# Kernel tuning notes

Measured on AMD Instinct MI355X. Metric: run time of the kernel, lower is better.

## Reference

```python
import jax, jax.numpy as jnp
import numpy as np


def setup_inputs() -> dict:
    key = jax.random.key(0)
    ks = jax.random.split(key, 16)
    B, S, L2 = 16, 1024, 2048

    def rn(k, shape, scale=0.1):
        return jax.random.normal(k, shape, dtype=jnp.float32) * scale

    return {
        "x": rn(ks[0], (B, S, 3), 1.0),
        "v1": rn(ks[1], (B, L2 + 1, 3), 1.0),
        "v2": rn(ks[2], (B, L2 + 1, 3), 1.0),
        # Attention: Linear(6, 1)
        "attn_w": rn(ks[3], (1, 6)),
        "attn_b": rn(ks[4], (1,)),
        # fc1: Linear(3, 16)
        "fc1_w": rn(ks[5], (16, 3)),
        "fc1_b": rn(ks[6], (16,)),
        # LSTM(16, 32, 1), gate order i,f,g,o -> 4*32 = 128
        "w_ih": rn(ks[7], (128, 16)),
        "w_hh": rn(ks[8], (128, 32)),
        "b_ih": rn(ks[9], (128,)),
        "b_hh": rn(ks[10], (128,)),
        # fc2: Linear(38, 16)
        "fc2_w": rn(ks[11], (16, 38)),
        "fc2_b": rn(ks[12], (16,)),
        # fc3: Linear(16, 3)
        "fc3_w": rn(ks[13], (3, 16)),
        "fc3_b": rn(ks[14], (3,)),
    }


def _attention(x, v, attn_w, attn_b):
    # Linear(6,1) over cat([x_i, key_j]) decomposes into x-part + key-part,
    # avoiding the original [B,S,L2,6] repeat/cat intermediate (same math).
    key_, value = v[:, :-1], v[:, 1:]          # [B,L2,3] each
    wx, wk = attn_w[0, :3], attn_w[0, 3:]
    scores = (x @ wx)[:, :, None] + (key_ @ wk)[:, None, :] + attn_b[0]  # [B,S,L2]
    a = jax.nn.softmax(scores, axis=-1)
    return jnp.einsum('bij,bjd->bid', a, value)  # [B,S,3]


def _lstm(x, w_ih, w_hh, b_ih, b_hh):
    # Single-layer batch_first LSTM, zero initial state, pytorch gate order i,f,g,o.
    B = x.shape[0]
    H = w_hh.shape[1]
    xg = x @ w_ih.T + (b_ih + b_hh)  # [B,S,4H] precomputed input contribution

    def step(carry, g_t):
        h, c = carry
        g = g_t + h @ w_hh.T
        i, f, gg, o = jnp.split(g, 4, axis=-1)
        c = jax.nn.sigmoid(f) * c + jax.nn.sigmoid(i) * jnp.tanh(gg)
        h = jax.nn.sigmoid(o) * jnp.tanh(c)
        return (h, c), h

    init = (jnp.zeros((B, H), x.dtype), jnp.zeros((B, H), x.dtype))
    _, hs = jax.lax.scan(step, init, jnp.swapaxes(xg, 0, 1))  # [S,B,H]
    return jnp.swapaxes(hs, 0, 1)  # [B,S,H]


def reference(x, v1, v2, attn_w, attn_b, fc1_w, fc1_b,
              w_ih, w_hh, b_ih, b_hh, fc2_w, fc2_b, fc3_w, fc3_b):
    a1 = _attention(x, v1, attn_w, attn_b)   # [B,S,3]
    a2 = _attention(x, v2, attn_w, attn_b)   # [B,S,3]
    h = _lstm(x @ fc1_w.T + fc1_b, w_ih, w_hh, b_ih, b_hh)  # [B,S,32]
    cat = jnp.concatenate([a1, a2, h], axis=-1)              # [B,S,38]
    out = jax.nn.relu(cat @ fc2_w.T + fc2_b) @ fc3_w.T + fc3_b
    return out  # [B,S,3]
```

## Files before the change

### kernel.cpp

```cpp
#include <hip/hip_runtime.h>
#include <hip/hip_bf16.h>

#define B_ 16
#define S_ 1024
#define L_ 2048
#define H_ 32

typedef float f2v __attribute__((ext_vector_type(2)));
typedef float f4v __attribute__((ext_vector_type(4)));

static __device__ __forceinline__ f2v pkfma(f2v a, f2v b, f2v c) {
    f2v d;
    asm("v_pk_fma_f32 %0, %1, %2, %3" : "=v"(d) : "v"(a), "v"(b), "v"(c));
    return d;
}
static __device__ __forceinline__ f2v pkadd(f2v a, f2v b) {
    f2v d;
    asm("v_pk_add_f32 %0, %1, %2" : "=v"(d) : "v"(a), "v"(b));
    return d;
}

__global__ __launch_bounds__(64) void fused_attn_lstm(
    const float* __restrict__ x,
    const float* __restrict__ v1,
    const float* __restrict__ v2,
    const float* __restrict__ attn_w,
    const float* __restrict__ fc1_w,
    const float* __restrict__ fc1_b,
    const float* __restrict__ w_ih,
    const float* __restrict__ w_hh,
    const float* __restrict__ b_ih,
    const float* __restrict__ b_hh,
    float* __restrict__ A,
    float* __restrict__ h_out)
{
    const int blk = blockIdx.x;
    const int l   = threadIdx.x;

    if (blk >= 16) {
        const int idx = blk - 16;
        const int b = idx & 15, sel = idx >> 4;
        const float* v = (sel ? v2 : v1) + (size_t)b * ((L_ + 1) * 3);
        const float wk0 = attn_w[3], wk1 = attn_w[4], wk2 = attn_w[5];

        float s[32];
        float mx = -3.4e38f;
#pragma unroll
        for (int k = 0; k < 32; ++k) {
            const float* p = v + (l + (k << 6)) * 3;
            float sc = fmaf(p[2], wk2, fmaf(p[1], wk1, p[0] * wk0));
            s[k] = sc; mx = fmaxf(mx, sc);
        }
#pragma unroll
        for (int o = 1; o < 64; o <<= 1) mx = fmaxf(mx, __shfl_xor(mx, o));

        float den = 0.f, a0 = 0.f, a1 = 0.f, a2 = 0.f;
#pragma unroll
        for (int k = 0; k < 32; ++k) {
            float e = __expf(s[k] - mx);
            const float* p = v + (l + (k << 6) + 1) * 3;
            den += e;
            a0 = fmaf(e, p[0], a0); a1 = fmaf(e, p[1], a1); a2 = fmaf(e, p[2], a2);
        }
#pragma unroll
        for (int o = 1; o < 64; o <<= 1) {
            den += __shfl_xor(den, o); a0 += __shfl_xor(a0, o);
            a1  += __shfl_xor(a1, o);  a2 += __shfl_xor(a2, o);
        }
        if (l == 0) {
            float inv = 1.0f / den;
            float* dst = A + sel * 48 + b * 3;
            dst[0] = a0 * inv; dst[1] = a1 * inv; dst[2] = a2 * inv;
        }
        return;
    }

    const int b  = blk;
    const int j  = l & 31;
    const int hi = l >> 5;
    const int r0 = hi ? (32 + j) : j;
    const int r1 = hi ? (96 + j) : (64 + j);

    __shared__ float lds_x[S_ * 3];
    __shared__ float lds_h[64];

    {
        const f4v* src = (const f4v*)(x + (size_t)b * (S_ * 3));
        f4v* dst = (f4v*)lds_x;
#pragma unroll
        for (int m = 0; m < 12; ++m) dst[l + 64 * m] = src[l + 64 * m];
    }
    if (l < 32) lds_h[l] = 0.f;

    f2v wh0[16], wh1[16];
    {
        const f4v* p0 = (const f4v*)(w_hh + r0 * H_);
        const f4v* p1 = (const f4v*)(w_hh + r1 * H_);
#pragma unroll
        for (int m = 0; m < 8; ++m) {
            f4v a = p0[m];
            wh0[2*m]   = __builtin_shufflevector(a, a, 0, 1);
            wh0[2*m+1] = __builtin_shufflevector(a, a, 2, 3);
            f4v c2 = p1[m];
            wh1[2*m]   = __builtin_shufflevector(c2, c2, 0, 1);
            wh1[2*m+1] = __builtin_shufflevector(c2, c2, 2, 3);
        }
    }

    float W00 = 0, W01 = 0, W02 = 0, W10 = 0, W11 = 0, W12 = 0, bb0, bb1;
    {
        float s0 = 0, s1 = 0;
#pragma unroll
        for (int k = 0; k < 16; ++k) {
            float wi0 = w_ih[r0 * 16 + k], wi1 = w_ih[r1 * 16 + k];
            float f0 = fc1_w[k * 3 + 0], f1 = fc1_w[k * 3 + 1], f2 = fc1_w[k * 3 + 2];
            float fb = fc1_b[k];
            W00 = fmaf(wi0, f0, W00); W01 = fmaf(wi0, f1, W01); W02 = fmaf(wi0, f2, W02);
            s0  = fmaf(wi0, fb, s0);
            W10 = fmaf(wi1, f0, W10); W11 = fmaf(wi1, f1, W11); W12 = fmaf(wi1, f2, W12);
            s1  = fmaf(wi1, fb, s1);
        }
        bb0 = s0 + b_ih[r0] + b_hh[r0];
        bb1 = s1 + b_ih[r1] + b_hh[r1];
    }

    const float CE = -1.44269504f;
    const float c1 = hi ? CE : 2.f * CE;
    float c = 0.f;
    float* hob = h_out + ((size_t)b << 15);

#define STEP(T, RB, WB) do {                                                          \
        float x0 = lds_x[3*(T)], x1 = lds_x[3*(T)+1], x2 = lds_x[3*(T)+2];            \
        f2v acc0a = { fmaf(W02,x2, fmaf(W01,x1, fmaf(W00,x0, bb0))), 0.f };           \
        f2v acc1a = { fmaf(W12,x2, fmaf(W11,x1, fmaf(W10,x0, bb1))), 0.f };           \
        f2v acc0b = { 0.f, 0.f };                                                     \
        f2v acc1b = { 0.f, 0.f };                                                     \
        _Pragma("unroll")                                                             \
        for (int m = 0; m < 8; ++m) {                                                 \
            f4v hv = *(const f4v*)&lds_h[(RB) + 4*m];                                 \
            f2v hlo = __builtin_shufflevector(hv, hv, 0, 1);                          \
            f2v hhi = __builtin_shufflevector(hv, hv, 2, 3);                          \
            acc0a = pkfma(wh0[2*m],   hlo, acc0a);                                    \
            acc1a = pkfma(wh1[2*m],   hlo, acc1a);                                    \
            acc0b = pkfma(wh0[2*m+1], hhi, acc0b);                                    \
            acc1b = pkfma(wh1[2*m+1], hhi, acc1b);                                    \
        }                                                                             \
        f2v acc0 = pkadd(acc0a, acc0b);                                               \
        f2v acc1 = pkadd(acc1a, acc1b);                                               \
        float a0 = acc0.x + acc0.y;                                                   \
        float a1 = acc1.x + acc1.y;                                                   \
        float s0 = __builtin_amdgcn_rcpf(1.f + __builtin_amdgcn_exp2f(a0 * CE));      \
        float s1 = __builtin_amdgcn_rcpf(1.f + __builtin_amdgcn_exp2f(a1 * c1));      \
        float t0 = __shfl_xor(s0, 32);                                                \
        float t1 = __shfl_xor(s1, 32);                                                \
        float si = hi ? t0 : s0;                                                      \
        float sf = hi ? s0 : t0;                                                      \
        float sg = hi ? t1 : s1;                                                      \
        float so = hi ? s1 : t1;                                                      \
        float tg = fmaf(2.f, sg, -1.f);                                               \
        c = fmaf(sf, c, si * tg);                                                     \
        float tc = fmaf(2.f, __builtin_amdgcn_rcpf(1.f + __builtin_amdgcn_exp2f(c * (2.f*CE))), -1.f); \
        float hval = so * tc;                                                         \
        if (!hi) lds_h[(WB) + j] = hval;                                              \
        else     hob[((T) << 5) + j] = hval;                                          \
    } while (0)

    for (int t = 0; t < S_; t += 2) {
        STEP(t,     0, 32);
        STEP(t + 1, 32, 0);
    }
#undef STEP
}

__global__ __launch_bounds__(256) void final_kernel(
    const float* __restrict__ h,
    const float* __restrict__ A,
    const float* __restrict__ fc2_w,
    const float* __restrict__ fc2_b,
    const float* __restrict__ fc3_w,
    const float* __restrict__ fc3_b,
    float* __restrict__ out)
{
    __shared__ float sw2[16 * 38], sb2[16], sw3[48], sb3[3], sA[96];
    const int tid = threadIdx.x;
    for (int i = tid; i < 16 * 38; i += 256) sw2[i] = fc2_w[i];
    if (tid < 96) sA[tid] = A[tid];
    if (tid < 16) sb2[tid] = fc2_b[tid];
    if (tid < 48) sw3[tid] = fc3_w[tid];
    if (tid < 3)  sb3[tid] = fc3_b[tid];
    __syncthreads();

    const int p = blockIdx.x * 256 + tid;
    if (p >= B_ * S_) return;
    const int b = p >> 10;

    float hv[32];
    {
        const float4* hp = (const float4*)(h + ((size_t)p << 5));
#pragma unroll
        for (int m = 0; m < 8; ++m) {
            float4 t = hp[m];
            hv[4*m] = t.x; hv[4*m+1] = t.y; hv[4*m+2] = t.z; hv[4*m+3] = t.w;
        }
    }
    const float a10 = sA[b*3+0], a11 = sA[b*3+1], a12 = sA[b*3+2];
    const float a20 = sA[48+b*3+0], a21 = sA[48+b*3+1], a22 = sA[48+b*3+2];

    float y[16];
#pragma unroll
    for (int u = 0; u < 16; ++u) {
        const float* w = sw2 + u * 38;
        float acc = sb2[u];
        acc = fmaf(w[0], a10, acc); acc = fmaf(w[1], a11, acc); acc = fmaf(w[2], a12, acc);
        acc = fmaf(w[3], a20, acc); acc = fmaf(w[4], a21, acc); acc = fmaf(w[5], a22, acc);
#pragma unroll
        for (int k = 0; k < 32; ++k) acc = fmaf(w[6 + k], hv[k], acc);
        y[u] = fmaxf(acc, 0.f);
    }
#pragma unroll
    for (int d = 0; d < 3; ++d) {
        float o = sb3[d];
#pragma unroll
        for (int u = 0; u < 16; ++u) o = fmaf(sw3[d * 16 + u], y[u], o);
        out[p * 3 + d] = o;
    }
}

extern "C" void kernel_launch(void* const* d_in, const int* in_sizes, int n_in,
                              void* d_out, int out_size, void* d_ws, size_t ws_size,
                              hipStream_t stream) {
    const float* x      = (const float*)d_in[0];
    const float* v1     = (const float*)d_in[1];
    const float* v2     = (const float*)d_in[2];
    const float* attn_w = (const float*)d_in[3];
    const float* fc1_w  = (const float*)d_in[5];
    const float* fc1_b  = (const float*)d_in[6];
    const float* w_ih   = (const float*)d_in[7];
    const float* w_hh   = (const float*)d_in[8];
    const float* b_ih   = (const float*)d_in[9];
    const float* b_hh   = (const float*)d_in[10];
    const float* fc2_w  = (const float*)d_in[11];
    const float* fc2_b  = (const float*)d_in[12];
    const float* fc3_w  = (const float*)d_in[13];
    const float* fc3_b  = (const float*)d_in[14];
    float* out = (float*)d_out;

    float* Aws = (float*)d_ws;
    float* hws = (float*)((char*)d_ws + 4096);

    fused_attn_lstm<<<48, 64, 0, stream>>>(x, v1, v2, attn_w, fc1_w, fc1_b,
                                           w_ih, w_hh, b_ih, b_hh, Aws, hws);
    final_kernel  <<<64, 256, 0, stream>>>(hws, Aws, fc2_w, fc2_b, fc3_w, fc3_b, out);
}
```

Before: 395.8 us.

## Fuse attention and output MLP into LSTM kernel, use permlane swap for gates

Merges the attention, LSTM and final MLP into one 16-block kernel, so the second launch and the attention workspace disappear. Each block now runs its two attention reductions and the fc2/fc3 epilogue after the recurrence. The log2e scaling is folded into the recurrent and input weights and biases, and the two cross-half shuffles per step become v_permlane32_swap. Both changes shorten the serial per-step dependency chain. The cost is that attention and the epilogue now run serially on only 16 wavefronts instead of in parallel blocks.

```diff
diff --git a/kernel.cpp b/kernel.cpp
--- a/kernel.cpp
+++ b/kernel.cpp
@@ -19,8 +19,11 @@
     asm("v_pk_add_f32 %0, %1, %2" : "=v"(d) : "v"(a), "v"(b));
     return d;
 }
-
-__global__ __launch_bounds__(64) void fused_attn_lstm(
+static __device__ __forceinline__ void pl32swap(float& a, float& b) {
+    asm("v_permlane32_swap_b32 %0, %1" : "+v"(a), "+v"(b));
+}
+
+__global__ __launch_bounds__(64) void fused_net(
     const float* __restrict__ x,
     const float* __restrict__ v1,
     const float* __restrict__ v2,
@@ -31,51 +34,15 @@
     const float* __restrict__ w_hh,
     const float* __restrict__ b_ih,
     const float* __restrict__ b_hh,
-    float* __restrict__ A,
-    float* __restrict__ h_out)
+    const float* __restrict__ fc2_w,
+    const float* __restrict__ fc2_b,
+    const float* __restrict__ fc3_w,
+    const float* __restrict__ fc3_b,
+    float* __restrict__ h_ws,
+    float* __restrict__ out)
 {
-    const int blk = blockIdx.x;
-    const int l   = threadIdx.x;
-
-    if (blk >= 16) {
-        const int idx = blk - 16;
-        const int b = idx & 15, sel = idx >> 4;
-        const float* v = (sel ? v2 : v1) + (size_t)b * ((L_ + 1) * 3);
-        const float wk0 = attn_w[3], wk1 = attn_w[4], wk2 = attn_w[5];
-
-        float s[32];
-        float mx = -3.4e38f;
-#pragma unroll
-        for (int k = 0; k < 32; ++k) {
-            const float* p = v + (l + (k << 6)) * 3;
-            float sc = fmaf(p[2], wk2, fmaf(p[1], wk1, p[0] * wk0));
-            s[k] = sc; mx = fmaxf(mx, sc);
-        }
-#pragma unroll
-        for (int o = 1; o < 64; o <<= 1) mx = fmaxf(mx, __shfl_xor(mx, o));
-
-        float den = 0.f, a0 = 0.f, a1 = 0.f, a2 = 0.f;
-#pragma unroll
-        for (int k = 0; k < 32; ++k) {
-            float e = __expf(s[k] - mx);
-            const float* p = v + (l + (k << 6) + 1) * 3;
-            den += e;
-            a0 = fmaf(e, p[0], a0); a1 = fmaf(e, p[1], a1); a2 = fmaf(e, p[2], a2);
-        }
-#pragma unroll
-        for (int o = 1; o < 64; o <<= 1) {
-            den += __shfl_xor(den, o); a0 += __shfl_xor(a0, o);
-            a1  += __shfl_xor(a1, o);  a2 += __shfl_xor(a2, o);
-        }
-        if (l == 0) {
-            float inv = 1.0f / den;
-            float* dst = A + sel * 48 + b * 3;
-            dst[0] = a0 * inv; dst[1] = a1 * inv; dst[2] = a2 * inv;
-        }
-        return;
-    }
-
-    const int b  = blk;
+    const int b  = blockIdx.x;
+    const int l  = threadIdx.x;
     const int j  = l & 31;
     const int hi = l >> 5;
     const int r0 = hi ? (32 + j) : j;
@@ -92,6 +59,9 @@
     }
     if (l < 32) lds_h[l] = 0.f;
 
+    const float CE = -1.44269504f;
+    const float k1 = hi ? CE : 2.f * CE;
+
     f2v wh0[16], wh1[16];
     {
         const f4v* p0 = (const f4v*)(w_hh + r0 * H_);
@@ -99,14 +69,13 @@
 #pragma unroll
         for (int m = 0; m < 8; ++m) {
             f4v a = p0[m];
-            wh0[2*m]   = __builtin_shufflevector(a, a, 0, 1);
-            wh0[2*m+1] = __builtin_shufflevector(a, a, 2, 3);
+            wh0[2*m]   = f2v{a.x * CE, a.y * CE};
+            wh0[2*m+1] = f2v{a.z * CE, a.w * CE};
             f4v c2 = p1[m];
-            wh1[2*m]   = __builtin_shufflevector(c2, c2, 0, 1);
-            wh1[2*m+1] = __builtin_shufflevector(c2, c2, 2, 3);
-        }
-    }
-
+            wh1[2*m]   = f2v{c2.x * k1, c2.y * k1};
+            wh1[2*m+1] = f2v{c2.z * k1, c2.w * k1};
+        }
+    }
     float W00 = 0, W01 = 0, W02 = 0, W10 = 0, W11 = 0, W12 = 0, bb0, bb1;
     {
         float s0 = 0, s1 = 0;
@@ -120,14 +89,14 @@
             W10 = fmaf(wi1, f0, W10); W11 = fmaf(wi1, f1, W11); W12 = fmaf(wi1, f2, W12);
             s1  = fmaf(wi1, fb, s1);
         }
-        bb0 = s0 + b_ih[r0] + b_hh[r0];
-        bb1 = s1 + b_ih[r1] + b_hh[r1];
-    }
-
-    const float CE = -1.44269504f;
-    const float c1 = hi ? CE : 2.f * CE;
+        bb0 = (s0 + b_ih[r0] + b_hh[r0]) * CE;
+        bb1 = (s1 + b_ih[r1] + b_hh[r1]) * k1;
+        W00 *= CE; W01 *= CE; W02 *= CE;
+        W10 *= k1; W11 *= k1; W12 *= k1;
+    }
+
     float c = 0.f;
-    float* hob = h_out + ((size_t)b << 15);
+    float* hob = h_ws + ((size_t)b << 15);
 
 #define STEP(T, RB, WB) do {                                                          \
         float x0 = lds_x[3*(T)], x1 = lds_x[3*(T)+1], x2 = lds_x[3*(T)+2];            \
@@ -147,16 +116,16 @@
         }                                                                             \
         f2v acc0 = pkadd(acc0a, acc0b);                                               \
         f2v acc1 = pkadd(acc1a, acc1b);                                               \
-        float a0 = acc0.x + acc0.y;                                                   \
-        float a1 = acc1.x + acc1.y;                                                   \
-        float s0 = __builtin_amdgcn_rcpf(1.f + __builtin_amdgcn_exp2f(a0 * CE));      \
-        float s1 = __builtin_amdgcn_rcpf(1.f + __builtin_amdgcn_exp2f(a1 * c1));      \
-        float t0 = __shfl_xor(s0, 32);                                                \
-        float t1 = __shfl_xor(s1, 32);                                                \
-        float si = hi ? t0 : s0;                                                      \
-        float sf = hi ? s0 : t0;                                                      \
-        float sg = hi ? t1 : s1;                                                      \
-        float so = hi ? s1 : t1;                                                      \
+        float s0 = __builtin_amdgcn_rcpf(1.f + __builtin_amdgcn_exp2f(acc0.x + acc0.y)); \
+        float s1 = __builtin_amdgcn_rcpf(1.f + __builtin_amdgcn_exp2f(acc1.x + acc1.y)); \
+        float A0 = s0, B0 = s1;                                                       \
+        pl32swap(A0, B0);                            \
+        float C0 = s1, D0 = s0;                                                       \
+        pl32swap(C0, D0);                            \
+        float si = hi ? C0 : s0;                                                      \
+        float sf = hi ? s0 : B0;                                                      \
+        float sg = hi ? A0 : s1;                                                      \
+        float so = hi ? s1 : D0;                                                      \
         float tg = fmaf(2.f, sg, -1.f);                                               \
         c = fmaf(sf, c, si * tg);                                                     \
         float tc = fmaf(2.f, __builtin_amdgcn_rcpf(1.f + __builtin_amdgcn_exp2f(c * (2.f*CE))), -1.f); \
@@ -170,59 +139,81 @@
         STEP(t + 1, 32, 0);
     }
 #undef STEP
-}
-
-__global__ __launch_bounds__(256) void final_kernel(
-    const float* __restrict__ h,
-    const float* __restrict__ A,
-    const float* __restrict__ fc2_w,
-    const float* __restrict__ fc2_b,
-    const float* __restrict__ fc3_w,
-    const float* __restrict__ fc3_b,
-    float* __restrict__ out)
-{
-    __shared__ float sw2[16 * 38], sb2[16], sw3[48], sb3[3], sA[96];
-    const int tid = threadIdx.x;
-    for (int i = tid; i < 16 * 38; i += 256) sw2[i] = fc2_w[i];
-    if (tid < 96) sA[tid] = A[tid];
-    if (tid < 16) sb2[tid] = fc2_b[tid];
-    if (tid < 48) sw3[tid] = fc3_w[tid];
-    if (tid < 3)  sb3[tid] = fc3_b[tid];
-    __syncthreads();
-
-    const int p = blockIdx.x * 256 + tid;
-    if (p >= B_ * S_) return;
-    const int b = p >> 10;
-
-    float hv[32];
-    {
-        const float4* hp = (const float4*)(h + ((size_t)p << 5));
-#pragma unroll
-        for (int m = 0; m < 8; ++m) {
-            float4 t = hp[m];
-            hv[4*m] = t.x; hv[4*m+1] = t.y; hv[4*m+2] = t.z; hv[4*m+3] = t.w;
-        }
-    }
-    const float a10 = sA[b*3+0], a11 = sA[b*3+1], a12 = sA[b*3+2];
-    const float a20 = sA[48+b*3+0], a21 = sA[48+b*3+1], a22 = sA[48+b*3+2];
-
-    float y[16];
-#pragma unroll
-    for (int u = 0; u < 16; ++u) {
-        const float* w = sw2 + u * 38;
-        float acc = sb2[u];
-        acc = fmaf(w[0], a10, acc); acc = fmaf(w[1], a11, acc); acc = fmaf(w[2], a12, acc);
-        acc = fmaf(w[3], a20, acc); acc = fmaf(w[4], a21, acc); acc = fmaf(w[5], a22, acc);
-#pragma unroll
-        for (int k = 0; k < 32; ++k) acc = fmaf(w[6 + k], hv[k], acc);
-        y[u] = fmaxf(acc, 0.f);
-    }
-#pragma unroll
-    for (int d = 0; d < 3; ++d) {
-        float o = sb3[d];
-#pragma unroll
-        for (int u = 0; u < 16; ++u) o = fmaf(sw3[d * 16 + u], y[u], o);
-        out[p * 3 + d] = o;
+
+    float a1v0, a1v1, a1v2, a2v0, a2v1, a2v2;
+    {
+        const float wk0 = attn_w[3], wk1 = attn_w[4], wk2 = attn_w[5];
+#pragma unroll
+        for (int sel = 0; sel < 2; ++sel) {
+            const float* v = (sel ? v2 : v1) + (size_t)b * ((L_ + 1) * 3);
+            float s[32];
+            float mx = -3.4e38f;
+#pragma unroll
+            for (int k = 0; k < 32; ++k) {
+                const float* p = v + (l + (k << 6)) * 3;
+                float sc = fmaf(p[2], wk2, fmaf(p[1], wk1, p[0] * wk0));
+                s[k] = sc; mx = fmaxf(mx, sc);
+            }
+#pragma unroll
+            for (int o = 1; o < 64; o <<= 1) mx = fmaxf(mx, __shfl_xor(mx, o));
+
+            float den = 0.f, a0 = 0.f, a1 = 0.f, a2 = 0.f;
+#pragma unroll
+            for (int k = 0; k < 32; ++k) {
+                float e = __expf(s[k] - mx);
+                const float* p = v + (l + (k << 6) + 1) * 3;
+                den += e;
+                a0 = fmaf(e, p[0], a0); a1 = fmaf(e, p[1], a1); a2 = fmaf(e, p[2], a2);
+            }
+#pragma unroll
+            for (int o = 1; o < 64; o <<= 1) {
+                den += __shfl_xor(den, o); a0 += __shfl_xor(a0, o);
+                a1  += __shfl_xor(a1, o);  a2 += __shfl_xor(a2, o);
+            }
+            float inv = 1.0f / den;
+            if (sel == 0) { a1v0 = a0 * inv; a1v1 = a1 * inv; a1v2 = a2 * inv; }
+            else          { a2v0 = a0 * inv; a2v1 = a1 * inv; a2v2 = a2 * inv; }
+        }
+    }
+
+    float* ldsw = lds_x;
+    for (int i = l; i < 608; i += 64) ldsw[i] = fc2_w[i];
+    if (l < 16) ldsw[608 + l] = fc2_b[l];
+    if (l < 48) ldsw[624 + l] = fc3_w[l];
+    if (l < 3)  ldsw[672 + l] = fc3_b[l];
+
+    const float* hrow = h_ws + ((size_t)b << 15);
+    float* orow = out + (size_t)b * (S_ * 3);
+#pragma unroll 1
+    for (int q = 0; q < 16; ++q) {
+        const int t = l + (q << 6);
+        float hv[32];
+        {
+            const f4v* hp = (const f4v*)(hrow + (t << 5));
+#pragma unroll
+            for (int m = 0; m < 8; ++m) {
+                f4v tv = hp[m];
+                hv[4*m] = tv.x; hv[4*m+1] = tv.y; hv[4*m+2] = tv.z; hv[4*m+3] = tv.w;
+            }
+        }
+        float y[16];
+#pragma unroll
+        for (int u = 0; u < 16; ++u) {
+            const float* w = ldsw + u * 38;
+            float acc = ldsw[608 + u];
+            acc = fmaf(w[0], a1v0, acc); acc = fmaf(w[1], a1v1, acc); acc = fmaf(w[2], a1v2, acc);
+            acc = fmaf(w[3], a2v0, acc); acc = fmaf(w[4], a2v1, acc); acc = fmaf(w[5], a2v2, acc);
+#pragma unroll
+            for (int k = 0; k < 32; ++k) acc = fmaf(w[6 + k], hv[k], acc);
+            y[u] = fmaxf(acc, 0.f);
+        }
+#pragma unroll
+        for (int d = 0; d < 3; ++d) {
+            float o = ldsw[672 + d];
+#pragma unroll
+            for (int u = 0; u < 16; ++u) o = fmaf(ldsw[624 + d * 16 + u], y[u], o);
+            orow[t * 3 + d] = o;
+        }
     }
 }
 
@@ -244,11 +235,9 @@
     const float* fc3_w  = (const float*)d_in[13];
     const float* fc3_b  = (const float*)d_in[14];
     float* out = (float*)d_out;
-
-    float* Aws = (float*)d_ws;
-    float* hws = (float*)((char*)d_ws + 4096);
-
-    fused_attn_lstm<<<48, 64, 0, stream>>>(x, v1, v2, attn_w, fc1_w, fc1_b,
-                                           w_ih, w_hh, b_ih, b_hh, Aws, hws);
-    final_kernel  <<<64, 256, 0, stream>>>(hws, Aws, fc2_w, fc2_b, fc3_w, fc3_b, out);
-}
+    float* hws = (float*)d_ws;
+
+    fused_net<<<16, 64, 0, stream>>>(x, v1, v2, attn_w, fc1_w, fc1_b,
+                                     w_ih, w_hh, b_ih, b_hh,
+                                     fc2_w, fc2_b, fc3_w, fc3_b, hws, out);
+}
```

New measurement: 421.9 us. 1.07x slower.
